# Kernel optimization log

Hardware: AMD Instinct MI355X
Metric: run time of the kernel (lower is better)

Reference implementation:

```python
import jax, jax.numpy as jnp
import numpy as np

B, T, D_IN = 1024, 128, 256
H = 128          # hidden_dim == memory_unit_size (required by einsum)
M = 128          # memory_units == memory_unit_size (required by view)
W = 128          # memory_unit_size
R = 4            # read_heads
OUT = 2


def setup_inputs() -> dict:
    key = jax.random.key(0)
    ks = jax.random.split(key, 9)
    s = 0.05
    return {
        "x": jax.random.normal(ks[0], (B, T, D_IN), dtype=jnp.float32),
        "memory": jax.random.normal(ks[1], (M, W), dtype=jnp.float32) * s,
        "read_vectors0": jax.random.normal(ks[2], (R, W), dtype=jnp.float32) * s,
        "W_ih": jax.random.normal(ks[3], (4 * H, D_IN + R * W), dtype=jnp.float32) * s,
        "W_hh": jax.random.normal(ks[4], (4 * H, H), dtype=jnp.float32) * s,
        "b_ih": jax.random.normal(ks[5], (4 * H,), dtype=jnp.float32) * s,
        "b_hh": jax.random.normal(ks[6], (4 * H,), dtype=jnp.float32) * s,
        "fc_w": jax.random.normal(ks[7], (OUT, H + R * W), dtype=jnp.float32) * s,
        "fc_b": jax.random.normal(ks[8], (OUT,), dtype=jnp.float32) * s,
    }


def reference(x, memory, read_vectors0, W_ih, W_hh, b_ih, b_hh, fc_w, fc_b):
    batch = x.shape[0]
    # softmax over memory slots (dim=0), constant across timesteps
    mem_sm = jax.nn.softmax(memory, axis=0)  # [M, W]
    bias = b_ih + b_hh

    # initial read vectors: [R, W] -> repeat over batch -> flatten [B, R*W]
    rv = jnp.tile(read_vectors0[None], (batch, 1, 1)).reshape(batch, R * W)
    h0 = jnp.zeros((batch, H), x.dtype)
    c0 = jnp.zeros((batch, H), x.dtype)

    def step(carry, xt):
        h, c, rv = carry
        inp = jnp.concatenate([xt, rv], axis=-1)           # [B, D_IN+R*W]
        gates = inp @ W_ih.T + h @ W_hh.T + bias           # [B, 4H]
        i, f, g, o = jnp.split(gates, 4, axis=-1)          # torch LSTM gate order
        c = jax.nn.sigmoid(f) * c + jax.nn.sigmoid(i) * jnp.tanh(g)
        h = jax.nn.sigmoid(o) * jnp.tanh(c)                # [B, H]
        read = jnp.einsum('ij,kj->ki', mem_sm, h)          # [B, M]
        # faithful to torch: repeat to [R, B, M] then view(B, R*M) (mixes rows)
        rv_new = jnp.broadcast_to(read[None], (R, batch, M)).reshape(batch, R * M)
        out = jnp.concatenate([h, rv_new], axis=-1) @ fc_w.T + fc_b  # [B, OUT]
        return (h, c, rv_new), out

    _, outs = jax.lax.scan(step, (h0, c0, rv), jnp.swapaxes(x, 0, 1))  # [T, B, OUT]
    return outs.mean(axis=0)  # [B, OUT]
```

## Files before the change

kernel.cpp:

```cpp
#include <hip/hip_runtime.h>

#define BB 1024
#define TT 128
#define NBLK 256

using bf16   = __bf16;
using bf16x8 = __attribute__((ext_vector_type(8))) bf16;
using bf16x4 = __attribute__((ext_vector_type(4))) bf16;
using f32x4  = __attribute__((ext_vector_type(4))) float;

__device__ __forceinline__ float fsig(float x) {
  return __builtin_amdgcn_rcpf(1.f + __expf(-x));
}
__device__ __forceinline__ float ftanh(float x) {
  return 2.f * __builtin_amdgcn_rcpf(1.f + __expf(-2.f * x)) - 1.f;
}

__device__ __forceinline__ void st_u32_coh(unsigned* p, unsigned v) {
  __hip_atomic_store(p, v, __ATOMIC_RELAXED, __HIP_MEMORY_SCOPE_AGENT);
}
__device__ __forceinline__ unsigned ld_u32_coh(const unsigned* p) {
  return __hip_atomic_load((unsigned*)p, __ATOMIC_RELAXED, __HIP_MEMORY_SCOPE_AGENT);
}
__device__ __forceinline__ float ld_f32_coh(const float* p) {
  return __hip_atomic_load((float*)p, __ATOMIC_RELAXED, __HIP_MEMORY_SCOPE_AGENT);
}
__device__ __forceinline__ void st_f32_coh(float* p, float v) {
  __hip_atomic_store(p, v, __ATOMIC_RELAXED, __HIP_MEMORY_SCOPE_AGENT);
}
__device__ __forceinline__ void st_u16_coh(unsigned short* p, unsigned short v) {
  __hip_atomic_store(p, v, __ATOMIC_RELAXED, __HIP_MEMORY_SCOPE_AGENT);
}
__device__ __forceinline__ bf16x8 ld_bf16x8_coh(const bf16* p) {
  union { unsigned long long u[2]; bf16x8 v; } c;
  c.u[0] = __hip_atomic_load((unsigned long long*)p, __ATOMIC_RELAXED, __HIP_MEMORY_SCOPE_AGENT);
  c.u[1] = __hip_atomic_load((unsigned long long*)(p + 4), __ATOMIC_RELAXED, __HIP_MEMORY_SCOPE_AGENT);
  return c.v;
}

__global__ void prep_a(const float* __restrict__ x, const float* __restrict__ mem,
                       const float* __restrict__ b_ih, const float* __restrict__ b_hh,
                       const float* __restrict__ rv0, const float* __restrict__ W_ih,
                       bf16* __restrict__ x_bf, float* __restrict__ mem_sm,
                       float* __restrict__ bias, float* __restrict__ G0,
                       unsigned* __restrict__ slots) {
  const int bid = blockIdx.x, tid = threadIdx.x;
  if (bid < 2048) {
    const int lane = tid & 63, wv = tid >> 6;
    const int wg = bid * 4 + wv;
#pragma unroll 4
    for (int r = 0; r < 16; ++r) {
      int rid = wg + r * 8192;
      int b = rid >> 7, t = rid & 127;
      int rowp = ((b >> 4) & 15) * 64 + (b >> 8) * 16 + (b & 15);
      const float4 v = *(const float4*)(x + (size_t)rid * 256 + lane * 4);
      bf16x4 o;
      o[0] = (bf16)v.x; o[1] = (bf16)v.y; o[2] = (bf16)v.z; o[3] = (bf16)v.w;
      *(bf16x4*)(x_bf + ((size_t)t * BB + rowp) * 256 + lane * 4) = o;
    }
  } else if (bid == 2048) {
    __shared__ float sM[128 * 128];
    for (int e = tid; e < 16384; e += 256) sM[e] = mem[e];
    __syncthreads();
    if (tid < 128) {
      float mx = -1e30f;
      for (int m = 0; m < 128; ++m) mx = fmaxf(mx, sM[m * 128 + tid]);
      float s = 0.f;
      for (int m = 0; m < 128; ++m) s += __expf(sM[m * 128 + tid] - mx);
      float inv = 1.f / s;
      for (int m = 0; m < 128; ++m) mem_sm[m * 128 + tid] = __expf(sM[m * 128 + tid] - mx) * inv;
    }
  } else if (bid == 2049) {
    for (int e = tid; e < 512; e += 256) bias[e] = b_ih[e] + b_hh[e];
  } else if (bid < 2052) {
    int g = (bid - 2050) * 256 + tid;
    float acc = 0.f;
    for (int k = 0; k < 512; ++k) acc += rv0[k] * W_ih[(size_t)g * 768 + 256 + k];
    G0[g] = acc;
  } else {
    for (int e = tid; e < 4096; e += 256) slots[e] = 0u;
  }
}

__global__ void prep_b(const float* __restrict__ W_ih, const float* __restrict__ fc_w,
                       const float* __restrict__ mem_sm,
                       bf16* __restrict__ WMg, float* __restrict__ FM) {
  const int bid = blockIdx.x, tid = threadIdx.x;
  if (bid < 512) {
    __shared__ float sW[512];
    const int g = bid;
    for (int e = tid; e < 512; e += 256) sW[e] = W_ih[(size_t)g * 768 + 256 + e];
    __syncthreads();
    const int r = tid >> 6, n0 = (tid & 63) * 2;
    float a0 = 0.f, a1 = 0.f;
    const float* wr = sW + r * 128;
#pragma unroll 4
    for (int m = 0; m < 128; ++m) {
      float2 ms = *(const float2*)(mem_sm + m * 128 + n0);
      a0 += wr[m] * ms.x;
      a1 += wr[m] * ms.y;
    }
    union { bf16 h[2]; unsigned u; } pk;
    pk.h[0] = (bf16)a0; pk.h[1] = (bf16)a1;
    *(unsigned*)(WMg + (size_t)g * 512 + r * 128 + n0) = pk.u;
  } else {
    for (int sub = tid; sub < 2 * 512; sub += 256) {
      int o = sub >> 9, rn = sub & 511, rr = rn >> 7, n = rn & 127;
      const float* wr = fc_w + o * 640 + 128 + rr * 128;
      float acc = 0.f;
      for (int m = 0; m < 128; ++m) acc += wr[m] * mem_sm[m * 128 + n];
      FM[o * 512 + rn] = acc;
    }
  }
}

__global__ void __launch_bounds__(256, 1) dnc_main(
    const bf16* __restrict__ x_bf, const bf16* __restrict__ WMg,
    const float* __restrict__ bias, const float* __restrict__ G0,
    const float* __restrict__ FM, bf16* __restrict__ hbuf0, bf16* __restrict__ hbuf1,
    float* __restrict__ hsumG, unsigned* __restrict__ slots,
    const float* __restrict__ W_ih, const float* __restrict__ W_hh,
    const float* __restrict__ fc_w, const float* __restrict__ fc_b,
    float* __restrict__ out) {
  __shared__ bf16 sWx[32][264];
  __shared__ bf16 sWhh[32][136];
  __shared__ bf16 sWM[32][520];
  __shared__ bf16 sHq[16][520];

  const int bid = blockIdx.x, tid = threadIdx.x;
  const int rt = bid >> 4, gt = bid & 15;
  const int wave = tid >> 6, lane = tid & 63;
  const int l15 = lane & 15, l4 = lane >> 4;

  auto gcol = [&](int pos) { return ((pos >> 3) << 7) + gt * 8 + (pos & 7); };

  for (int e = tid; e < 32 * 256; e += 256) sWx[e >> 8][e & 255] = (bf16)W_ih[(size_t)gcol(e >> 8) * 768 + (e & 255)];
  for (int e = tid; e < 32 * 128; e += 256) sWhh[e >> 7][e & 127] = (bf16)W_hh[gcol(e >> 7) * 128 + (e & 127)];
  for (int e = tid; e < 32 * 512; e += 256) sWM[e >> 9][e & 511] = WMg[(size_t)gcol(e >> 9) * 512 + (e & 511)];
  __syncthreads();

  const float bv0 = bias[gcol(l15)], bv1 = bias[gcol(16 + l15)];

  const bool lo = (l15 < 8);
  const int j = l15 & 7;
  const int rb = lo ? 0 : 2;
  float cst[2] = {0.f, 0.f}, hsum[2] = {0.f, 0.f};
  int growp[2];
#pragma unroll
  for (int k = 0; k < 2; ++k) growp[k] = rt * 16 + (l4 * 4 + rb + k) + 256 * wave;

  f32x4 acc0, acc1;

  auto xpart = [&](int t) {
    acc0 = f32x4{bv0, bv0, bv0, bv0};
    acc1 = f32x4{bv1, bv1, bv1, bv1};
    const bf16* xr = x_bf + ((size_t)t * BB + rt * 64 + wave * 16 + l15) * 256 + l4 * 8;
#pragma unroll
    for (int kk = 0; kk < 8; ++kk) {
      bf16x8 a  = *(const bf16x8*)(xr + kk * 32);
      bf16x8 w0 = *(const bf16x8*)&sWx[l15][kk * 32 + l4 * 8];
      bf16x8 w1 = *(const bf16x8*)&sWx[16 + l15][kk * 32 + l4 * 8];
      acc0 = __builtin_amdgcn_mfma_f32_16x16x32_bf16(a, w0, acc0, 0, 0, 0);
      acc1 = __builtin_amdgcn_mfma_f32_16x16x32_bf16(a, w1, acc1, 0, 0, 0);
    }
  };

  auto hpart = [&](const bf16* hrd) {
    bf16x8 ha[4];
    const bf16* hr = hrd + (size_t)(rt * 16 + l15 + 256 * wave) * 128 + l4 * 8;
#pragma unroll
    for (int kk = 0; kk < 4; ++kk) ha[kk] = ld_bf16x8_coh(hr + kk * 32);
#pragma unroll
    for (int pass = 0; pass < 4; ++pass) {
      int row = (tid >> 4) + 16 * pass, seg = tid & 15;
      bf16x8 v = ld_bf16x8_coh(hrd + (size_t)(rt * 64 + row) * 128 + seg * 8);
      *(bf16x8*)&sHq[row >> 2][(row & 3) * 128 + seg * 8] = v;
    }
#pragma unroll
    for (int kk = 0; kk < 4; ++kk) {
      bf16x8 w0 = *(const bf16x8*)&sWhh[l15][kk * 32 + l4 * 8];
      bf16x8 w1 = *(const bf16x8*)&sWhh[16 + l15][kk * 32 + l4 * 8];
      acc0 = __builtin_amdgcn_mfma_f32_16x16x32_bf16(ha[kk], w0, acc0, 0, 0, 0);
      acc1 = __builtin_amdgcn_mfma_f32_16x16x32_bf16(ha[kk], w1, acc1, 0, 0, 0);
    }
    __syncthreads();
#pragma unroll
    for (int kk = 0; kk < 16; ++kk) {
      bf16x8 a  = *(const bf16x8*)&sHq[l15][kk * 32 + l4 * 8];
      bf16x8 w0 = *(const bf16x8*)&sWM[l15][kk * 32 + l4 * 8];
      bf16x8 w1 = *(const bf16x8*)&sWM[16 + l15][kk * 32 + l4 * 8];
      acc0 = __builtin_amdgcn_mfma_f32_16x16x32_bf16(a, w0, acc0, 0, 0, 0);
      acc1 = __builtin_amdgcn_mfma_f32_16x16x32_bf16(a, w1, acc1, 0, 0, 0);
    }
  };

  auto pw = [&](bool add_g0, bf16* hwr) {
    float o0[4], o1[4];
#pragma unroll
    for (int r = 0; r < 4; ++r) {
      o0[r] = __shfl_xor(acc0[r], 8);
      o1[r] = __shfl_xor(acc1[r], 8);
    }
    float g0i = 0.f, g0f = 0.f, g0g = 0.f, g0o = 0.f;
    if (add_g0) {
      int cb = gt * 8 + j;
      g0i = G0[cb]; g0f = G0[128 + cb]; g0g = G0[256 + cb]; g0o = G0[384 + cb];
    }
#pragma unroll
    for (int k = 0; k < 2; ++k) {
      int r = rb + k;
      float gi = (lo ? acc0[r] : o0[r]) + g0i;
      float gf = (lo ? o0[r] : acc0[r]) + g0f;
      float gg = (lo ? acc1[r] : o1[r]) + g0g;
      float go = (lo ? o1[r] : acc1[r]) + g0o;
      cst[k] = fsig(gf) * cst[k] + fsig(gi) * ftanh(gg);
      float h = fsig(go) * ftanh(cst[k]);
      hsum[k] += h;
      union { bf16 b; unsigned short u; } cv; cv.b = (bf16)h;
      st_u16_coh((unsigned short*)(hwr + (size_t)growp[k] * 128 + gt * 8 + j), cv.u);
    }
  };

  auto commit = [&](unsigned gen) {
    asm volatile("s_waitcnt vmcnt(0)" ::: "memory");
    __syncthreads();
    if (tid == 0) st_u32_coh(slots + bid * 16, gen);
  };
  auto gridwait = [&](unsigned gen) {
    while (ld_u32_coh(slots + tid * 16) < gen) {}
    __syncthreads();
  };

  xpart(0);
  pw(true, hbuf0);
  commit(1);
  for (int t = 1; t < TT; ++t) {
    xpart(t);
    gridwait(t);
    hpart((t & 1) ? hbuf0 : hbuf1);
    pw(false, (t & 1) ? hbuf1 : hbuf0);
    commit(t + 1);
  }
#pragma unroll
  for (int k = 0; k < 2; ++k)
    st_f32_coh(hsumG + (size_t)growp[k] * 128 + gt * 8 + j, hsum[k]);
  commit(TT + 1);
  gridwait(TT + 1);
  {
    int row = bid * 4 + wave;
    const float* hsr = hsumG + (size_t)row * 128;
    const float* hqr = hsumG + (size_t)(row & 255) * 512;
    float s0 = 0.f, s1 = 0.f;
    for (int k = lane; k < 128; k += 64) { float v = ld_f32_coh(hsr + k); s0 += v * fc_w[k]; s1 += v * fc_w[640 + k]; }
    for (int k = lane; k < 512; k += 64) { float v = ld_f32_coh(hqr + k); s0 += v * FM[k]; s1 += v * FM[512 + k]; }
    for (int off = 32; off > 0; off >>= 1) { s0 += __shfl_down(s0, off); s1 += __shfl_down(s1, off); }
    if (lane == 0) {
      out[row * 2 + 0] = s0 * (1.f / 128.f) + fc_b[0];
      out[row * 2 + 1] = s1 * (1.f / 128.f) + fc_b[1];
    }
  }
}

extern "C" void kernel_launch(void* const* d_in, const int* in_sizes, int n_in,
                              void* d_out, int out_size, void* d_ws, size_t ws_size,
                              hipStream_t stream) {
  const float* x      = (const float*)d_in[0];
  const float* memory = (const float*)d_in[1];
  const float* rv0    = (const float*)d_in[2];
  const float* W_ih   = (const float*)d_in[3];
  const float* W_hh   = (const float*)d_in[4];
  const float* b_ih   = (const float*)d_in[5];
  const float* b_hh   = (const float*)d_in[6];
  const float* fc_w   = (const float*)d_in[7];
  const float* fc_b   = (const float*)d_in[8];
  float* out = (float*)d_out;
  char* ws = (char*)d_ws;

  bf16*     x_bf   = (bf16*)ws;
  bf16*     WMg    = (bf16*)(ws + 67108864);
  float*    mem_sm = (float*)(ws + 67633152);
  float*    bias   = (float*)(ws + 67698688);
  float*    G0     = (float*)(ws + 67700736);
  float*    FM     = (float*)(ws + 67702784);
  bf16*     hbuf0  = (bf16*)(ws + 67706880);
  bf16*     hbuf1  = (bf16*)(ws + 67969024);
  unsigned* slots  = (unsigned*)(ws + 68231168);
  float*    hsumG  = (float*)(ws + 68247552);

  prep_a<<<2053, 256, 0, stream>>>(x, memory, b_ih, b_hh, rv0, W_ih,
                                   x_bf, mem_sm, bias, G0, slots);
  prep_b<<<513, 256, 0, stream>>>(W_ih, fc_w, mem_sm, WMg, FM);
  dnc_main<<<NBLK, 256, 0, stream>>>(x_bf, WMg, bias, G0, FM, hbuf0, hbuf1, hsumG, slots,
                                     W_ih, W_hh, fc_w, fc_b, out);
}
```

Baseline: 841.0 us.

## Replace per-step grid barrier with poison-flagged per-timestep h buffers

Instead of a grid-wide flag barrier each timestep on double-buffered h, every timestep writes h into its own buffer that is pre-filled with a NaN poison pattern. Consumers spin on the loaded values until none still holds poison, so each block waits only for the h rows it needs. The separate x bf16 transpose pass is dropped and x is read as fp32 and converted inside the main loop. This grows the h workspace to hold all timesteps and depends on a real h value never matching the poison bit pattern.

Result: slower. 916.7 us (+9.0%).

```diff
diff --git a/kernel.cpp b/kernel.cpp
--- a/kernel.cpp
+++ b/kernel.cpp
@@ -3,10 +3,10 @@
 #define BB 1024
 #define TT 128
 #define NBLK 256
+#define POISON64 0x7FC07FC07FC07FC0ULL
 
 using bf16   = __bf16;
 using bf16x8 = __attribute__((ext_vector_type(8))) bf16;
-using bf16x4 = __attribute__((ext_vector_type(4))) bf16;
 using f32x4  = __attribute__((ext_vector_type(4))) float;
 
 __device__ __forceinline__ float fsig(float x) {
@@ -31,44 +31,36 @@
 __device__ __forceinline__ void st_u16_coh(unsigned short* p, unsigned short v) {
   __hip_atomic_store(p, v, __ATOMIC_RELAXED, __HIP_MEMORY_SCOPE_AGENT);
 }
-__device__ __forceinline__ bf16x8 ld_bf16x8_coh(const bf16* p) {
-  union { unsigned long long u[2]; bf16x8 v; } c;
-  c.u[0] = __hip_atomic_load((unsigned long long*)p, __ATOMIC_RELAXED, __HIP_MEMORY_SCOPE_AGENT);
-  c.u[1] = __hip_atomic_load((unsigned long long*)(p + 4), __ATOMIC_RELAXED, __HIP_MEMORY_SCOPE_AGENT);
-  return c.v;
-}
-
-__global__ void prep_a(const float* __restrict__ x, const float* __restrict__ mem,
+__device__ __forceinline__ unsigned long long ld_u64_coh(const void* p) {
+  return __hip_atomic_load((unsigned long long*)p, __ATOMIC_RELAXED, __HIP_MEMORY_SCOPE_AGENT);
+}
+__device__ __forceinline__ bool haspoison(unsigned long long v) {
+  unsigned long long x = v ^ POISON64;
+  return ((x - 0x0001000100010001ULL) & ~x & 0x8000800080008000ULL) != 0ULL;
+}
+
+__global__ void prep_a(const float* __restrict__ mem,
                        const float* __restrict__ b_ih, const float* __restrict__ b_hh,
                        const float* __restrict__ rv0, const float* __restrict__ W_ih,
-                       bf16* __restrict__ x_bf, float* __restrict__ mem_sm,
+                       bf16* __restrict__ hbufs, float* __restrict__ mem_sm,
                        float* __restrict__ bias, float* __restrict__ G0,
                        unsigned* __restrict__ slots) {
   const int bid = blockIdx.x, tid = threadIdx.x;
   if (bid < 2048) {
-    const int lane = tid & 63, wv = tid >> 6;
-    const int wg = bid * 4 + wv;
-#pragma unroll 4
-    for (int r = 0; r < 16; ++r) {
-      int rid = wg + r * 8192;
-      int b = rid >> 7, t = rid & 127;
-      int rowp = ((b >> 4) & 15) * 64 + (b >> 8) * 16 + (b & 15);
-      const float4 v = *(const float4*)(x + (size_t)rid * 256 + lane * 4);
-      bf16x4 o;
-      o[0] = (bf16)v.x; o[1] = (bf16)v.y; o[2] = (bf16)v.z; o[3] = (bf16)v.w;
-      *(bf16x4*)(x_bf + ((size_t)t * BB + rowp) * 256 + lane * 4) = o;
+    char* base = (char*)hbufs + (size_t)bid * 16384 + tid * 16;
+#pragma unroll
+    for (int ps = 0; ps < 4; ++ps) {
+      unsigned long long* p = (unsigned long long*)(base + ps * 4096);
+      p[0] = POISON64; p[1] = POISON64;
     }
   } else if (bid == 2048) {
-    __shared__ float sM[128 * 128];
-    for (int e = tid; e < 16384; e += 256) sM[e] = mem[e];
-    __syncthreads();
     if (tid < 128) {
       float mx = -1e30f;
-      for (int m = 0; m < 128; ++m) mx = fmaxf(mx, sM[m * 128 + tid]);
+      for (int m = 0; m < 128; ++m) mx = fmaxf(mx, mem[m * 128 + tid]);
       float s = 0.f;
-      for (int m = 0; m < 128; ++m) s += __expf(sM[m * 128 + tid] - mx);
+      for (int m = 0; m < 128; ++m) s += __expf(mem[m * 128 + tid] - mx);
       float inv = 1.f / s;
-      for (int m = 0; m < 128; ++m) mem_sm[m * 128 + tid] = __expf(sM[m * 128 + tid] - mx) * inv;
+      for (int m = 0; m < 128; ++m) mem_sm[m * 128 + tid] = __expf(mem[m * 128 + tid] - mx) * inv;
     }
   } else if (bid == 2049) {
     for (int e = tid; e < 512; e += 256) bias[e] = b_ih[e] + b_hh[e];
@@ -115,9 +107,9 @@
 }
 
 __global__ void __launch_bounds__(256, 1) dnc_main(
-    const bf16* __restrict__ x_bf, const bf16* __restrict__ WMg,
+    const float* __restrict__ x, const bf16* __restrict__ WMg,
     const float* __restrict__ bias, const float* __restrict__ G0,
-    const float* __restrict__ FM, bf16* __restrict__ hbuf0, bf16* __restrict__ hbuf1,
+    const float* __restrict__ FM, bf16* __restrict__ hbufs,
     float* __restrict__ hsumG, unsigned* __restrict__ slots,
     const float* __restrict__ W_ih, const float* __restrict__ W_hh,
     const float* __restrict__ fc_w, const float* __restrict__ fc_b,
@@ -149,15 +141,21 @@
 #pragma unroll
   for (int k = 0; k < 2; ++k) growp[k] = rt * 16 + (l4 * 4 + rb + k) + 256 * wave;
 
+  const float* xrow = x + (size_t)(rt * 16 + l15 + 256 * wave) * (TT * 256);
+
   f32x4 acc0, acc1;
 
   auto xpart = [&](int t) {
     acc0 = f32x4{bv0, bv0, bv0, bv0};
     acc1 = f32x4{bv1, bv1, bv1, bv1};
-    const bf16* xr = x_bf + ((size_t)t * BB + rt * 64 + wave * 16 + l15) * 256 + l4 * 8;
+    const float* xr = xrow + (size_t)t * 256 + l4 * 8;
 #pragma unroll
     for (int kk = 0; kk < 8; ++kk) {
-      bf16x8 a  = *(const bf16x8*)(xr + kk * 32);
+      float4 u0 = *(const float4*)(xr + kk * 32);
+      float4 u1 = *(const float4*)(xr + kk * 32 + 4);
+      bf16x8 a;
+      a[0] = (bf16)u0.x; a[1] = (bf16)u0.y; a[2] = (bf16)u0.z; a[3] = (bf16)u0.w;
+      a[4] = (bf16)u1.x; a[5] = (bf16)u1.y; a[6] = (bf16)u1.z; a[7] = (bf16)u1.w;
       bf16x8 w0 = *(const bf16x8*)&sWx[l15][kk * 32 + l4 * 8];
       bf16x8 w1 = *(const bf16x8*)&sWx[16 + l15][kk * 32 + l4 * 8];
       acc0 = __builtin_amdgcn_mfma_f32_16x16x32_bf16(a, w0, acc0, 0, 0, 0);
@@ -166,22 +164,45 @@
   };
 
   auto hpart = [&](const bf16* hrd) {
-    bf16x8 ha[4];
-    const bf16* hr = hrd + (size_t)(rt * 16 + l15 + 256 * wave) * 128 + l4 * 8;
-#pragma unroll
-    for (int kk = 0; kk < 4; ++kk) ha[kk] = ld_bf16x8_coh(hr + kk * 32);
+    const bf16* hr  = hrd + (size_t)(rt * 16 + l15 + 256 * wave) * 128 + l4 * 8;
+    const bf16* hs0 = hrd + (size_t)(rt * 64 + (tid >> 4)) * 128 + (tid & 15) * 8;
+    unsigned long long v[16];
+#pragma unroll
+    for (int i = 0; i < 16; ++i) {
+      const bf16* p = (i < 8) ? (hr + (i >> 1) * 32 + (i & 1) * 4)
+                              : (hs0 + (size_t)((i - 8) >> 1) * 2048 + (i & 1) * 4);
+      v[i] = ld_u64_coh(p);
+    }
+    for (;;) {
+      unsigned stale = 0;
+#pragma unroll
+      for (int i = 0; i < 16; ++i) stale |= haspoison(v[i]) ? (1u << i) : 0u;
+      if (!stale) break;
+      __builtin_amdgcn_s_sleep(1);
+#pragma unroll
+      for (int i = 0; i < 16; ++i)
+        if (stale & (1u << i)) {
+          const bf16* p = (i < 8) ? (hr + (i >> 1) * 32 + (i & 1) * 4)
+                                  : (hs0 + (size_t)((i - 8) >> 1) * 2048 + (i & 1) * 4);
+          v[i] = ld_u64_coh(p);
+        }
+    }
+#pragma unroll
+    for (int kk = 0; kk < 4; ++kk) {
+      union { unsigned long long u[2]; bf16x8 b; } c;
+      c.u[0] = v[2 * kk]; c.u[1] = v[2 * kk + 1];
+      bf16x8 w0 = *(const bf16x8*)&sWhh[l15][kk * 32 + l4 * 8];
+      bf16x8 w1 = *(const bf16x8*)&sWhh[16 + l15][kk * 32 + l4 * 8];
+      acc0 = __builtin_amdgcn_mfma_f32_16x16x32_bf16(c.b, w0, acc0, 0, 0, 0);
+      acc1 = __builtin_amdgcn_mfma_f32_16x16x32_bf16(c.b, w1, acc1, 0, 0, 0);
+    }
+    __syncthreads();
 #pragma unroll
     for (int pass = 0; pass < 4; ++pass) {
       int row = (tid >> 4) + 16 * pass, seg = tid & 15;
-      bf16x8 v = ld_bf16x8_coh(hrd + (size_t)(rt * 64 + row) * 128 + seg * 8);
-      *(bf16x8*)&sHq[row >> 2][(row & 3) * 128 + seg * 8] = v;
-    }
-#pragma unroll
-    for (int kk = 0; kk < 4; ++kk) {
-      bf16x8 w0 = *(const bf16x8*)&sWhh[l15][kk * 32 + l4 * 8];
-      bf16x8 w1 = *(const bf16x8*)&sWhh[16 + l15][kk * 32 + l4 * 8];
-      acc0 = __builtin_amdgcn_mfma_f32_16x16x32_bf16(ha[kk], w0, acc0, 0, 0, 0);
-      acc1 = __builtin_amdgcn_mfma_f32_16x16x32_bf16(ha[kk], w1, acc1, 0, 0, 0);
+      union { unsigned long long u[2]; bf16x8 b; } c;
+      c.u[0] = v[8 + 2 * pass]; c.u[1] = v[9 + 2 * pass];
+      *(bf16x8*)&sHq[row >> 2][(row & 3) * 128 + seg * 8] = c.b;
     }
     __syncthreads();
 #pragma unroll
@@ -232,20 +253,17 @@
   };
 
   xpart(0);
-  pw(true, hbuf0);
-  commit(1);
+  pw(true, hbufs);
   for (int t = 1; t < TT; ++t) {
     xpart(t);
-    gridwait(t);
-    hpart((t & 1) ? hbuf0 : hbuf1);
-    pw(false, (t & 1) ? hbuf1 : hbuf0);
-    commit(t + 1);
+    hpart(hbufs + (size_t)(t - 1) * (BB * 128));
+    pw(false, hbufs + (size_t)t * (BB * 128));
   }
 #pragma unroll
   for (int k = 0; k < 2; ++k)
     st_f32_coh(hsumG + (size_t)growp[k] * 128 + gt * 8 + j, hsum[k]);
-  commit(TT + 1);
-  gridwait(TT + 1);
+  commit(1);
+  gridwait(1);
   {
     int row = bid * 4 + wave;
     const float* hsr = hsumG + (size_t)row * 128;
@@ -276,20 +294,18 @@
   float* out = (float*)d_out;
   char* ws = (char*)d_ws;
 
-  bf16*     x_bf   = (bf16*)ws;
-  bf16*     WMg    = (bf16*)(ws + 67108864);
-  float*    mem_sm = (float*)(ws + 67633152);
-  float*    bias   = (float*)(ws + 67698688);
-  float*    G0     = (float*)(ws + 67700736);
-  float*    FM     = (float*)(ws + 67702784);
-  bf16*     hbuf0  = (bf16*)(ws + 67706880);
-  bf16*     hbuf1  = (bf16*)(ws + 67969024);
-  unsigned* slots  = (unsigned*)(ws + 68231168);
-  float*    hsumG  = (float*)(ws + 68247552);
-
-  prep_a<<<2053, 256, 0, stream>>>(x, memory, b_ih, b_hh, rv0, W_ih,
-                                   x_bf, mem_sm, bias, G0, slots);
+  bf16*     hbufs  = (bf16*)ws;
+  bf16*     WMg    = (bf16*)(ws + 33554432);
+  float*    mem_sm = (float*)(ws + 34078720);
+  float*    bias   = (float*)(ws + 34144256);
+  float*    G0     = (float*)(ws + 34146304);
+  float*    FM     = (float*)(ws + 34148352);
+  unsigned* slots  = (unsigned*)(ws + 34152448);
+  float*    hsumG  = (float*)(ws + 34168832);
+
+  prep_a<<<2053, 256, 0, stream>>>(memory, b_ih, b_hh, rv0, W_ih,
+                                   hbufs, mem_sm, bias, G0, slots);
   prep_b<<<513, 256, 0, stream>>>(W_ih, fc_w, mem_sm, WMg, FM);
-  dnc_main<<<NBLK, 256, 0, stream>>>(x_bf, WMg, bias, G0, FM, hbuf0, hbuf1, hsumG, slots,
+  dnc_main<<<NBLK, 256, 0, stream>>>(x, WMg, bias, G0, FM, hbufs, hsumG, slots,
                                      W_ih, W_hh, fc_w, fc_b, out);
 }
```

## Replace grid-wide barrier with per-wave dependency flags and merge prep kernels

Applied to the files above, without the earlier changes.

The per-timestep grid barrier, where every block waited on all 256 block slots, becomes per-wave signals. Each block now waits only on the producer waves whose h rows it reads, tracked by the row mixing of the read vectors. The h buffer ring grows from 2 to 4 entries so faster blocks can run ahead without overwriting data still being read. The two prep kernels merge into one launch, with each WM block recomputing the memory softmax redundantly, and hsumG reuses the x_bf workspace region. The risk is subtle ordering or aliasing bugs, since hsumG overlaps x_bf while other blocks may still be reading x.

New measurement: 924.4 us. 9.9% more time.

```diff
diff --git a/kernel.cpp b/kernel.cpp
--- a/kernel.cpp
+++ b/kernel.cpp
@@ -38,12 +38,13 @@
   return c.v;
 }
 
-__global__ void prep_a(const float* __restrict__ x, const float* __restrict__ mem,
-                       const float* __restrict__ b_ih, const float* __restrict__ b_hh,
-                       const float* __restrict__ rv0, const float* __restrict__ W_ih,
-                       bf16* __restrict__ x_bf, float* __restrict__ mem_sm,
-                       float* __restrict__ bias, float* __restrict__ G0,
-                       unsigned* __restrict__ slots) {
+__global__ void prep(const float* __restrict__ x, const float* __restrict__ mem,
+                     const float* __restrict__ b_ih, const float* __restrict__ b_hh,
+                     const float* __restrict__ rv0, const float* __restrict__ W_ih,
+                     const float* __restrict__ fc_w,
+                     bf16* __restrict__ x_bf, bf16* __restrict__ WMg,
+                     float* __restrict__ bias, float* __restrict__ G0,
+                     float* __restrict__ FM, unsigned* __restrict__ slots) {
   const int bid = blockIdx.x, tid = threadIdx.x;
   if (bid < 2048) {
     const int lane = tid & 63, wv = tid >> 6;
@@ -58,22 +59,53 @@
       o[0] = (bf16)v.x; o[1] = (bf16)v.y; o[2] = (bf16)v.z; o[3] = (bf16)v.w;
       *(bf16x4*)(x_bf + ((size_t)t * BB + rowp) * 256 + lane * 4) = o;
     }
-  } else if (bid == 2048) {
-    __shared__ float sM[128 * 128];
-    for (int e = tid; e < 16384; e += 256) sM[e] = mem[e];
-    __syncthreads();
+  } else if (bid < 2560) {
+    __shared__ float sSM[16384];
+    const int g = bid - 2048;
     if (tid < 128) {
       float mx = -1e30f;
-      for (int m = 0; m < 128; ++m) mx = fmaxf(mx, sM[m * 128 + tid]);
+      for (int m = 0; m < 128; ++m) mx = fmaxf(mx, mem[m * 128 + tid]);
       float s = 0.f;
-      for (int m = 0; m < 128; ++m) s += __expf(sM[m * 128 + tid] - mx);
+      for (int m = 0; m < 128; ++m) s += __expf(mem[m * 128 + tid] - mx);
       float inv = 1.f / s;
-      for (int m = 0; m < 128; ++m) mem_sm[m * 128 + tid] = __expf(sM[m * 128 + tid] - mx) * inv;
-    }
-  } else if (bid == 2049) {
+      for (int m = 0; m < 128; ++m) sSM[m * 128 + tid] = __expf(mem[m * 128 + tid] - mx) * inv;
+    }
+    __syncthreads();
+    const int r = tid >> 6, n0 = (tid & 63) * 2;
+    const float* wr = W_ih + (size_t)g * 768 + 256 + r * 128;
+    float a0 = 0.f, a1 = 0.f;
+#pragma unroll 4
+    for (int m = 0; m < 128; ++m) {
+      float2 ms = *(const float2*)(sSM + m * 128 + n0);
+      float w = wr[m];
+      a0 += w * ms.x;
+      a1 += w * ms.y;
+    }
+    union { bf16 h[2]; unsigned u; } pk;
+    pk.h[0] = (bf16)a0; pk.h[1] = (bf16)a1;
+    *(unsigned*)(WMg + (size_t)g * 512 + r * 128 + n0) = pk.u;
+  } else if (bid == 2560) {
+    __shared__ float sSM[16384];
+    if (tid < 128) {
+      float mx = -1e30f;
+      for (int m = 0; m < 128; ++m) mx = fmaxf(mx, mem[m * 128 + tid]);
+      float s = 0.f;
+      for (int m = 0; m < 128; ++m) s += __expf(mem[m * 128 + tid] - mx);
+      float inv = 1.f / s;
+      for (int m = 0; m < 128; ++m) sSM[m * 128 + tid] = __expf(mem[m * 128 + tid] - mx) * inv;
+    }
+    __syncthreads();
+    for (int sub = tid; sub < 2 * 512; sub += 256) {
+      int o = sub >> 9, rn = sub & 511, rr = rn >> 7, n = rn & 127;
+      const float* wr = fc_w + o * 640 + 128 + rr * 128;
+      float acc = 0.f;
+      for (int m = 0; m < 128; ++m) acc += wr[m] * sSM[m * 128 + n];
+      FM[o * 512 + rn] = acc;
+    }
+  } else if (bid == 2561) {
     for (int e = tid; e < 512; e += 256) bias[e] = b_ih[e] + b_hh[e];
-  } else if (bid < 2052) {
-    int g = (bid - 2050) * 256 + tid;
+  } else if (bid < 2564) {
+    int g = (bid - 2562) * 256 + tid;
     float acc = 0.f;
     for (int k = 0; k < 512; ++k) acc += rv0[k] * W_ih[(size_t)g * 768 + 256 + k];
     G0[g] = acc;
@@ -82,42 +114,10 @@
   }
 }
 
-__global__ void prep_b(const float* __restrict__ W_ih, const float* __restrict__ fc_w,
-                       const float* __restrict__ mem_sm,
-                       bf16* __restrict__ WMg, float* __restrict__ FM) {
-  const int bid = blockIdx.x, tid = threadIdx.x;
-  if (bid < 512) {
-    __shared__ float sW[512];
-    const int g = bid;
-    for (int e = tid; e < 512; e += 256) sW[e] = W_ih[(size_t)g * 768 + 256 + e];
-    __syncthreads();
-    const int r = tid >> 6, n0 = (tid & 63) * 2;
-    float a0 = 0.f, a1 = 0.f;
-    const float* wr = sW + r * 128;
-#pragma unroll 4
-    for (int m = 0; m < 128; ++m) {
-      float2 ms = *(const float2*)(mem_sm + m * 128 + n0);
-      a0 += wr[m] * ms.x;
-      a1 += wr[m] * ms.y;
-    }
-    union { bf16 h[2]; unsigned u; } pk;
-    pk.h[0] = (bf16)a0; pk.h[1] = (bf16)a1;
-    *(unsigned*)(WMg + (size_t)g * 512 + r * 128 + n0) = pk.u;
-  } else {
-    for (int sub = tid; sub < 2 * 512; sub += 256) {
-      int o = sub >> 9, rn = sub & 511, rr = rn >> 7, n = rn & 127;
-      const float* wr = fc_w + o * 640 + 128 + rr * 128;
-      float acc = 0.f;
-      for (int m = 0; m < 128; ++m) acc += wr[m] * mem_sm[m * 128 + n];
-      FM[o * 512 + rn] = acc;
-    }
-  }
-}
-
 __global__ void __launch_bounds__(256, 1) dnc_main(
     const bf16* __restrict__ x_bf, const bf16* __restrict__ WMg,
     const float* __restrict__ bias, const float* __restrict__ G0,
-    const float* __restrict__ FM, bf16* __restrict__ hbuf0, bf16* __restrict__ hbuf1,
+    const float* __restrict__ FM, bf16* __restrict__ hbufs,
     float* __restrict__ hsumG, unsigned* __restrict__ slots,
     const float* __restrict__ W_ih, const float* __restrict__ W_hh,
     const float* __restrict__ fc_w, const float* __restrict__ fc_b,
@@ -148,6 +148,8 @@
   int growp[2];
 #pragma unroll
   for (int k = 0; k < 2; ++k) growp[k] = rt * 16 + (l4 * 4 + rb + k) + 256 * wave;
+
+  auto hb = [&](int t) { return hbufs + (size_t)(t & 3) * (BB * 128); };
 
   f32x4 acc0, acc1;
 
@@ -221,31 +223,37 @@
     }
   };
 
-  auto commit = [&](unsigned gen) {
+  auto signal = [&](unsigned gen) {
     asm volatile("s_waitcnt vmcnt(0)" ::: "memory");
+    if (lane == 0) st_u32_coh(slots + (bid * 4 + wave) * 4, gen);
+  };
+  auto waitdeps = [&](unsigned gen) {
+    if (tid < 128) {
+      int s;
+      if (tid < 64) s = (rt * 16 + (tid & 15)) * 4 + (tid >> 4);
+      else          s = ((4 * (rt & 3) + ((tid >> 4) & 3)) * 16 + (tid & 15)) * 4 + (rt >> 2);
+      while (ld_u32_coh(slots + s * 4) < gen) {}
+    }
     __syncthreads();
-    if (tid == 0) st_u32_coh(slots + bid * 16, gen);
-  };
-  auto gridwait = [&](unsigned gen) {
-    while (ld_u32_coh(slots + tid * 16) < gen) {}
-    __syncthreads();
   };
 
   xpart(0);
-  pw(true, hbuf0);
-  commit(1);
+  pw(true, hb(0));
+  signal(1);
   for (int t = 1; t < TT; ++t) {
     xpart(t);
-    gridwait(t);
-    hpart((t & 1) ? hbuf0 : hbuf1);
-    pw(false, (t & 1) ? hbuf1 : hbuf0);
-    commit(t + 1);
+    waitdeps(t);
+    hpart(hb(t - 1));
+    pw(false, hb(t));
+    signal(t + 1);
   }
 #pragma unroll
   for (int k = 0; k < 2; ++k)
     st_f32_coh(hsumG + (size_t)growp[k] * 128 + gt * 8 + j, hsum[k]);
-  commit(TT + 1);
-  gridwait(TT + 1);
+  signal(TT + 2);
+  for (int k = tid; k < 1024; k += 256)
+    while (ld_u32_coh(slots + k * 4) < TT + 2) {}
+  __syncthreads();
   {
     int row = bid * 4 + wave;
     const float* hsr = hsumG + (size_t)row * 128;
@@ -278,18 +286,15 @@
 
   bf16*     x_bf   = (bf16*)ws;
   bf16*     WMg    = (bf16*)(ws + 67108864);
-  float*    mem_sm = (float*)(ws + 67633152);
   float*    bias   = (float*)(ws + 67698688);
   float*    G0     = (float*)(ws + 67700736);
   float*    FM     = (float*)(ws + 67702784);
-  bf16*     hbuf0  = (bf16*)(ws + 67706880);
-  bf16*     hbuf1  = (bf16*)(ws + 67969024);
-  unsigned* slots  = (unsigned*)(ws + 68231168);
-  float*    hsumG  = (float*)(ws + 68247552);
-
-  prep_a<<<2053, 256, 0, stream>>>(x, memory, b_ih, b_hh, rv0, W_ih,
-                                   x_bf, mem_sm, bias, G0, slots);
-  prep_b<<<513, 256, 0, stream>>>(W_ih, fc_w, mem_sm, WMg, FM);
-  dnc_main<<<NBLK, 256, 0, stream>>>(x_bf, WMg, bias, G0, FM, hbuf0, hbuf1, hsumG, slots,
+  bf16*     hbufs  = (bf16*)(ws + 67706880);
+  unsigned* slots  = (unsigned*)(ws + 68755456);
+  float*    hsumG  = (float*)ws;
+
+  prep<<<2565, 256, 0, stream>>>(x, memory, b_ih, b_hh, rv0, W_ih, fc_w,
+                                 x_bf, WMg, bias, G0, FM, slots);
+  dnc_main<<<NBLK, 256, 0, stream>>>(x_bf, WMg, bias, G0, FM, hbufs, hsumG, slots,
                                      W_ih, W_hh, fc_w, fc_b, out);
 }
```
